# Performance work log

Measured on AMD Instinct MI355X. Metric: run time of the kernel, lower is better.

Reference implementation:

```python
import jax, jax.numpy as jnp
import numpy as np

B, N, D_IN, D_OUT, H = 4, 512, 1024, 1024, 16
HD = D_IN // H      # key head dim (FAISS k_features)
VD = D_OUT // H     # value head dim
MEM = 32768         # memory_size per head
IPQ = 8             # items_per_query
SCALE = HD ** -0.5


def setup_inputs() -> dict:
    key = jax.random.key(0)
    ks = jax.random.split(key, 9)
    s = 0.02
    return {
        "x": jax.random.normal(ks[0], (B, N, D_IN), jnp.float32),
        "Wq": jax.random.normal(ks[1], (D_IN, D_IN), jnp.float32) * s,
        "Wk": jax.random.normal(ks[2], (D_IN, D_IN), jnp.float32) * s,
        "Wv": jax.random.normal(ks[3], (D_OUT, D_IN), jnp.float32) * s,
        "Ww": jax.random.normal(ks[4], (D_OUT, D_IN), jnp.float32) * s,
        "Wo": jax.random.normal(ks[5], (D_OUT, D_OUT), jnp.float32) * s,
        "bo": jnp.zeros((D_OUT,), jnp.float32),
        "k_mem0": jax.random.normal(ks[6], (H, MEM, HD), jnp.float32) * s,
        "v_mem0": jax.random.normal(ks[7], (H, MEM, VD), jnp.float32) * s,
    }


def _attention(q, k, v, Wo, bo):
    # q: [b,n,D_IN], k: [b,m,D_IN], v: [b,m,D_OUT]
    b, n, _ = q.shape
    m = k.shape[1]
    qh = q.reshape(b, n, H, HD)
    kh = k.reshape(b, m, H, HD)
    vh = v.reshape(b, m, H, VD)
    sim = jnp.einsum("bihd,bjhd->bhij", qh, kh) * SCALE
    att = jax.nn.softmax(sim, axis=-1)
    out = jnp.einsum("bhij,bjhd->bihd", att, vh).reshape(b, n, H * VD)
    return out @ Wo.T + bo


def reference(x, Wq, Wk, Wv, Ww, Wo, bo, k_mem0, v_mem0):
    b, n, _ = x.shape
    q = x @ Wq.T          # [b,n,D_IN]
    k = x @ Wk.T          # [b,n,D_IN]
    v = x @ Wv.T          # [b,n,D_OUT]
    w = jax.nn.sigmoid(x @ Ww.T)

    a = _attention(q, k, v, Wo, bo)

    # per-head flat views: [h, b*n, hd]
    qh = q.reshape(b, n, H, HD).transpose(2, 0, 1, 3).reshape(H, b * n, HD)
    kh = k.reshape(b, n, H, HD).transpose(2, 0, 1, 3).reshape(H, b * n, HD)
    vh = v.reshape(b, n, H, VD).transpose(2, 0, 1, 3).reshape(H, b * n, VD)

    m_ins = b * n
    # FIFO insert: drop oldest m_ins rows, append new keys/values
    k_mem = jnp.concatenate([k_mem0[:, m_ins:], kh], axis=1)  # [h, MEM, HD]
    v_mem = jnp.concatenate([v_mem0[:, m_ins:], vh], axis=1)  # [h, MEM, VD]

    # exact inner-product search (IndexFlatIP), top IPQ per query, per head
    sims = jnp.einsum("hqd,hmd->hqm", qh, k_mem)               # [h, b*n, MEM]
    _, idx = jax.lax.top_k(sims, IPQ)                          # [h, b*n, IPQ]
    idx = idx.reshape(H, b * n * IPQ, 1)
    k_ret = jnp.take_along_axis(k_mem, idx, axis=1)            # [h, b*n*IPQ, HD]
    v_ret = jnp.take_along_axis(v_mem, idx, axis=1)            # [h, b*n*IPQ, VD]

    # 'h (b m) hd -> b m (h hd)' with m = n*IPQ
    k_m = k_ret.reshape(H, b, n * IPQ, HD).transpose(1, 2, 0, 3).reshape(b, n * IPQ, D_IN)
    v_m = v_ret.reshape(H, b, n * IPQ, VD).transpose(1, 2, 0, 3).reshape(b, n * IPQ, D_OUT)

    a_m = _attention(q, k_m, v_m, Wo, bo)
    return w * a + (1.0 - w) * a_m
```

## Files before the change

kernel.cpp:

```cpp
#include <hip/hip_runtime.h>
#include <float.h>
#include <math.h>


#define DIN   1024
#define NHEADS 16
#define HD    64
#define NB    4
#define NSEQ  512
#define BN    2048
#define MEMN  32768
#define OLDN  30720
#define IPQ   8
#define ATT_SCALE 0.125f
#define SZ    (BN * DIN)

typedef __attribute__((ext_vector_type(4))) float floatx4;
typedef __attribute__((ext_vector_type(8))) short short8;

__device__ __forceinline__ unsigned short f2bf(float f) {
    unsigned int u = __float_as_uint(f);
    return (unsigned short)((u + 0x7FFFu + ((u >> 16) & 1u)) >> 16);
}
__device__ __forceinline__ float bf2f(unsigned short s) {
    return __uint_as_float(((unsigned int)s) << 16);
}
__device__ __forceinline__ unsigned cvt_pk_bf16(float a, float b) {
    unsigned r;
    asm("v_cvt_pk_bf16_f32 %0, %1, %2" : "=v"(r) : "v"(a), "v"(b));
    return r;
}
__device__ __forceinline__ void split_pack(float4 a, float4 b, short8 &hi, short8 &lo) {
    float v[8] = {a.x, a.y, a.z, a.w, b.x, b.y, b.z, b.w};
    union { unsigned u[4]; short8 s; } H, L;
#pragma unroll
    for (int j = 0; j < 4; ++j) {
        unsigned h = cvt_pk_bf16(v[2 * j], v[2 * j + 1]);
        float r0 = v[2 * j]     - __uint_as_float(h << 16);
        float r1 = v[2 * j + 1] - __uint_as_float(h & 0xFFFF0000u);
        H.u[j] = h;
        L.u[j] = cvt_pk_bf16(r0, r1);
    }
    hi = H.s; lo = L.s;
}
__device__ __forceinline__ floatx4 mfma16(short8 a, short8 b, floatx4 c) {
    return __builtin_amdgcn_mfma_f32_16x16x32_bf16(a, b, c, 0, 0, 0);
}

__global__ void init_kernel(unsigned int* nrm) {
    if (threadIdx.x < NHEADS) nrm[threadIdx.x] = 0u;
}

__global__ __launch_bounds__(256) void gemm_mfma(
    const float* __restrict__ A,
    const float* __restrict__ W0, const float* __restrict__ W1,
    const float* __restrict__ W2, const float* __restrict__ W3,
    float* __restrict__ C0, float* __restrict__ C1,
    float* __restrict__ C2, float* __restrict__ C3,
    int sigmoidZ)
{
    __shared__ short Ahi_s[128 * 32];
    __shared__ short Alo_s[128 * 32];
    __shared__ short Bhi_s[128 * 32];
    __shared__ short Blo_s[128 * 32];

    int z = blockIdx.z;
    const float* W = (z == 0) ? W0 : (z == 1) ? W1 : (z == 2) ? W2 : W3;
    float* C = (z == 0) ? C0 : (z == 1) ? C1 : (z == 2) ? C2 : C3;

    int tid = threadIdx.x;
    int wv = tid >> 6, lane = tid & 63, quad = lane >> 4, l16 = lane & 15;
    int row0 = blockIdx.y * 128, col0 = blockIdx.x * 128;
    int wm = (wv >> 1) * 64, wn = (wv & 1) * 64;

    floatx4 zero4 = {0.f, 0.f, 0.f, 0.f};
    floatx4 acc[4][4];
#pragma unroll
    for (int i = 0; i < 4; ++i)
#pragma unroll
        for (int j = 0; j < 4; ++j) acc[i][j] = zero4;

    for (int kk = 0; kk < DIN; kk += 32) {
        __syncthreads();
#pragma unroll
        for (int p = 0; p < 2; ++p) {
            int g = tid * 2 + p;
            int row = g >> 2, cc = (g & 3) * 8;
            const float* ap = A + (size_t)(row0 + row) * DIN + kk + cc;
            float4 a0 = *(const float4*)ap;
            float4 a1 = *(const float4*)(ap + 4);
            short8 h8, l8;
            split_pack(a0, a1, h8, l8);
            *(short8*)&Ahi_s[g * 8] = h8;
            *(short8*)&Alo_s[g * 8] = l8;
            const float* bp = W + (size_t)(col0 + row) * DIN + kk + cc;
            float4 b0 = *(const float4*)bp;
            float4 b1 = *(const float4*)(bp + 4);
            split_pack(b0, b1, h8, l8);
            *(short8*)&Bhi_s[g * 8] = h8;
            *(short8*)&Blo_s[g * 8] = l8;
        }
        __syncthreads();

        short8 ah[4], al[4], bh[4], bl[4];
#pragma unroll
        for (int t = 0; t < 4; ++t) {
            int ar = (wm + t * 16 + l16) * 32 + quad * 8;
            int br = (wn + t * 16 + l16) * 32 + quad * 8;
            ah[t] = *(const short8*)&Ahi_s[ar];
            al[t] = *(const short8*)&Alo_s[ar];
            bh[t] = *(const short8*)&Bhi_s[br];
            bl[t] = *(const short8*)&Blo_s[br];
        }
#pragma unroll
        for (int tm = 0; tm < 4; ++tm)
#pragma unroll
            for (int tn = 0; tn < 4; ++tn) {
                floatx4 c = acc[tm][tn];
                c = mfma16(al[tm], bl[tn], c);
                c = mfma16(al[tm], bh[tn], c);
                c = mfma16(ah[tm], bl[tn], c);
                c = mfma16(ah[tm], bh[tn], c);
                acc[tm][tn] = c;
            }
    }

    bool sig = (sigmoidZ == z);
#pragma unroll
    for (int tm = 0; tm < 4; ++tm)
#pragma unroll
        for (int tn = 0; tn < 4; ++tn)
#pragma unroll
            for (int r = 0; r < 4; ++r) {
                int row = row0 + wm + tm * 16 + quad * 4 + r;
                int col = col0 + wn + tn * 16 + l16;
                float vv = acc[tm][tn][r];
                if (sig) vv = 1.f / (1.f + __expf(-vv));
                C[(size_t)row * DIN + col] = vv;
            }
}

__global__ __launch_bounds__(256) void oldnorm_kernel(
    const float* __restrict__ kmem0, unsigned int* __restrict__ nrm)
{
    int h = blockIdx.y;
    int c0 = blockIdx.x * 1024;
    int part = threadIdx.x & 15, rg = threadIdx.x >> 4;
    const float* base = kmem0 + ((size_t)h * MEMN + BN) * HD;
    float mx = 0.f;
    for (int it = 0; it < 64; ++it) {
        int row = c0 + it * 16 + rg;
        float4 vv = *(const float4*)(base + (size_t)row * HD + part * 4);
        float s = vv.x * vv.x + vv.y * vv.y + vv.z * vv.z + vv.w * vv.w;
#pragma unroll
        for (int o = 1; o < 16; o <<= 1) s += __shfl_xor(s, o, 16);
        mx = fmaxf(mx, s);
    }
    __shared__ float red[256];
    red[threadIdx.x] = mx;
    __syncthreads();
    for (int st = 128; st > 0; st >>= 1) {
        if (threadIdx.x < st) red[threadIdx.x] = fmaxf(red[threadIdx.x], red[threadIdx.x + st]);
        __syncthreads();
    }
    if (threadIdx.x == 0) atomicMax(nrm + h, __float_as_uint(sqrtf(red[0])));
}

__device__ __forceinline__ void insert_top8(float (&tv)[8], int (&ti)[8], float v, int id) {
    if (v < tv[7] || (v == tv[7] && id > ti[7])) return;
    tv[7] = v; ti[7] = id;
#pragma unroll
    for (int s = 7; s > 0; --s) {
        bool sw = (tv[s] > tv[s - 1]) || (tv[s] == tv[s - 1] && ti[s] < ti[s - 1]);
        if (sw) {
            float fv = tv[s]; tv[s] = tv[s - 1]; tv[s - 1] = fv;
            int iv = ti[s]; ti[s] = ti[s - 1]; ti[s - 1] = iv;
        }
    }
}

__global__ __launch_bounds__(256, 2) void search_kernel(
    const float* __restrict__ q, const float* __restrict__ knew,
    const float* __restrict__ kmem0, const unsigned int* __restrict__ nrm,
    int* __restrict__ idxOut)
{
    __shared__ short Khi[32 * 72];
    __shared__ short Klo[32 * 72];
    __shared__ int sflag;
    int tid = threadIdx.x;
    int qt = blockIdx.x, h = blockIdx.y;
    int wv = tid >> 6, lane = tid & 63, quad = lane >> 4, l16 = lane & 15;
    if (tid == 0) sflag = 0;

    short8 qhi[2], qlo[2];
    float qn2;
    {
        int qrow = qt * 64 + wv * 16 + l16;
        const float* qp = q + (size_t)qrow * DIN + h * HD;
        float sq = 0.f;
#pragma unroll
        for (int st = 0; st < 2; ++st) {
            float4 a = *(const float4*)(qp + st * 32 + quad * 8);
            float4 c = *(const float4*)(qp + st * 32 + quad * 8 + 4);
            sq += a.x * a.x + a.y * a.y + a.z * a.z + a.w * a.w
                + c.x * c.x + c.y * c.y + c.z * c.z + c.w * c.w;
            split_pack(a, c, qhi[st], qlo[st]);
        }
        sq += __shfl_xor(sq, 16);
        sq += __shfl_xor(sq, 32);
        qn2 = sq;
    }

    float tv[4][8]; int ti[4][8];
#pragma unroll
    for (int r = 0; r < 4; ++r)
#pragma unroll
        for (int s = 0; s < 8; ++s) { tv[r][s] = -FLT_MAX; ti[r][s] = 0x7FFFFFFF; }

    for (int ch = 0; ch < 64; ++ch) {
        __syncthreads();
        {
            int key = tid >> 3, part = tid & 7;
            const float* kr = knew + (size_t)(ch * 32 + key) * DIN + h * HD;
            float4 ka = *(const float4*)(kr + part * 8);
            float4 kb = *(const float4*)(kr + part * 8 + 4);
            short8 kh8, kl8;
            split_pack(ka, kb, kh8, kl8);
            *(short8*)&Khi[key * 72 + part * 8] = kh8;
            *(short8*)&Klo[key * 72 + part * 8] = kl8;
        }
        __syncthreads();

        short8 kh00 = *(const short8*)&Khi[l16 * 72 + quad * 8];
        short8 kh01 = *(const short8*)&Khi[l16 * 72 + 32 + quad * 8];
        short8 kl00 = *(const short8*)&Klo[l16 * 72 + quad * 8];
        short8 kl01 = *(const short8*)&Klo[l16 * 72 + 32 + quad * 8];
        short8 kh10 = *(const short8*)&Khi[(16 + l16) * 72 + quad * 8];
        short8 kh11 = *(const short8*)&Khi[(16 + l16) * 72 + 32 + quad * 8];
        short8 kl10 = *(const short8*)&Klo[(16 + l16) * 72 + quad * 8];
        short8 kl11 = *(const short8*)&Klo[(16 + l16) * 72 + 32 + quad * 8];
        floatx4 zero4 = {0.f, 0.f, 0.f, 0.f};
        floatx4 s0 = zero4, s1 = zero4;
        s0 = mfma16(qhi[0], kh00, s0); s0 = mfma16(qhi[1], kh01, s0);
        s0 = mfma16(qlo[0], kh00, s0); s0 = mfma16(qlo[1], kh01, s0);
        s0 = mfma16(qhi[0], kl00, s0); s0 = mfma16(qhi[1], kl01, s0);
        s1 = mfma16(qhi[0], kh10, s1); s1 = mfma16(qhi[1], kh11, s1);
        s1 = mfma16(qlo[0], kh10, s1); s1 = mfma16(qlo[1], kh11, s1);
        s1 = mfma16(qhi[0], kl10, s1); s1 = mfma16(qhi[1], kl11, s1);

        int base = OLDN + ch * 32;
#pragma unroll
        for (int r = 0; r < 4; ++r) {
            insert_top8(tv[r], ti[r], s0[r], base + l16);
            insert_top8(tv[r], ti[r], s1[r], base + 16 + l16);
        }
    }

    float val8[4], keepv[4];
    int keepi[4];
#pragma unroll
    for (int rr = 0; rr < 4; ++rr) { keepv[rr] = -FLT_MAX; keepi[rr] = 0x7FFFFFFF; val8[rr] = -FLT_MAX; }
#pragma unroll
    for (int rr = 0; rr < 4; ++rr) {
#pragma unroll
        for (int m = 0; m < 8; ++m) {
            float cv = tv[rr][0]; int ci = ti[rr][0];
#pragma unroll
            for (int o = 1; o < 16; o <<= 1) {
                float ov = __shfl_xor(cv, o, 16);
                int oi = __shfl_xor(ci, o, 16);
                if (ov > cv || (ov == cv && oi < ci)) { cv = ov; ci = oi; }
            }
            if (tv[rr][0] == cv && ti[rr][0] == ci) {
#pragma unroll
                for (int s = 0; s < 7; ++s) { tv[rr][s] = tv[rr][s + 1]; ti[rr][s] = ti[rr][s + 1]; }
                tv[rr][7] = -FLT_MAX; ti[rr][7] = 0x7FFFFFFF;
            }
            if (l16 == m) { keepv[rr] = cv; keepi[rr] = ci; }
            if (l16 == 0)
                idxOut[((size_t)h * BN + qt * 64 + wv * 16 + quad * 4 + rr) * IPQ + m] = ci;
            val8[rr] = cv;
        }
    }

    float oldMax = __uint_as_float(nrm[h]);
    bool need = false;
#pragma unroll
    for (int rr = 0; rr < 4; ++rr) {
        float bq = __shfl(qn2, quad * 4 + rr, 16);
        float bnd = sqrtf(bq) * oldMax * 1.0001f + 1e-5f;
        if (bnd >= val8[rr]) need = true;
    }
    if (need) sflag = 1;
    __syncthreads();

    if (sflag) {
#pragma unroll
        for (int rr = 0; rr < 4; ++rr) {
            tv[rr][0] = (l16 < 8) ? keepv[rr] : -FLT_MAX;
            ti[rr][0] = (l16 < 8) ? keepi[rr] : 0x7FFFFFFF;
#pragma unroll
            for (int s = 1; s < 8; ++s) { tv[rr][s] = -FLT_MAX; ti[rr][s] = 0x7FFFFFFF; }
        }
        for (int ch = 0; ch < 960; ++ch) {
            __syncthreads();
            {
                int key = tid >> 3, part = tid & 7;
                const float* kr = kmem0 + ((size_t)h * MEMN + BN + ch * 32 + key) * HD;
                float4 ka = *(const float4*)(kr + part * 8);
                float4 kb = *(const float4*)(kr + part * 8 + 4);
                short8 kh8, kl8;
                split_pack(ka, kb, kh8, kl8);
                *(short8*)&Khi[key * 72 + part * 8] = kh8;
                *(short8*)&Klo[key * 72 + part * 8] = kl8;
            }
            __syncthreads();

            short8 kh00 = *(const short8*)&Khi[l16 * 72 + quad * 8];
            short8 kh01 = *(const short8*)&Khi[l16 * 72 + 32 + quad * 8];
            short8 kl00 = *(const short8*)&Klo[l16 * 72 + quad * 8];
            short8 kl01 = *(const short8*)&Klo[l16 * 72 + 32 + quad * 8];
            short8 kh10 = *(const short8*)&Khi[(16 + l16) * 72 + quad * 8];
            short8 kh11 = *(const short8*)&Khi[(16 + l16) * 72 + 32 + quad * 8];
            short8 kl10 = *(const short8*)&Klo[(16 + l16) * 72 + quad * 8];
            short8 kl11 = *(const short8*)&Klo[(16 + l16) * 72 + 32 + quad * 8];
            floatx4 zero4 = {0.f, 0.f, 0.f, 0.f};
            floatx4 s0 = zero4, s1 = zero4;
            s0 = mfma16(qhi[0], kh00, s0); s0 = mfma16(qhi[1], kh01, s0);
            s0 = mfma16(qlo[0], kh00, s0); s0 = mfma16(qlo[1], kh01, s0);
            s0 = mfma16(qhi[0], kl00, s0); s0 = mfma16(qhi[1], kl01, s0);
            s1 = mfma16(qhi[0], kh10, s1); s1 = mfma16(qhi[1], kh11, s1);
            s1 = mfma16(qlo[0], kh10, s1); s1 = mfma16(qlo[1], kh11, s1);
            s1 = mfma16(qhi[0], kl10, s1); s1 = mfma16(qhi[1], kl11, s1);

            int base = ch * 32;
#pragma unroll
            for (int r = 0; r < 4; ++r) {
                insert_top8(tv[r], ti[r], s0[r], base + l16);
                insert_top8(tv[r], ti[r], s1[r], base + 16 + l16);
            }
        }
#pragma unroll
        for (int rr = 0; rr < 4; ++rr) {
#pragma unroll
            for (int m = 0; m < 8; ++m) {
                float cv = tv[rr][0]; int ci = ti[rr][0];
#pragma unroll
                for (int o = 1; o < 16; o <<= 1) {
                    float ov = __shfl_xor(cv, o, 16);
                    int oi = __shfl_xor(ci, o, 16);
                    if (ov > cv || (ov == cv && oi < ci)) { cv = ov; ci = oi; }
                }
                if (tv[rr][0] == cv && ti[rr][0] == ci) {
#pragma unroll
                    for (int s = 0; s < 7; ++s) { tv[rr][s] = tv[rr][s + 1]; ti[rr][s] = ti[rr][s + 1]; }
                    tv[rr][7] = -FLT_MAX; ti[rr][7] = 0x7FFFFFFF;
                }
                if (l16 == 0)
                    idxOut[((size_t)h * BN + qt * 64 + wv * 16 + quad * 4 + rr) * IPQ + m] = ci;
            }
        }
    }
}

__global__ __launch_bounds__(256, 2) void attn_kernel(
    const float* __restrict__ q, const float* __restrict__ knew,
    const float* __restrict__ vnew, const float* __restrict__ kmem0,
    const float* __restrict__ vmem0, const int* __restrict__ idxb,
    float* __restrict__ AO, float* __restrict__ G)
{
    __shared__ short Khi[32 * 72];
    __shared__ short Klo[32 * 72];
    __shared__ short Vthi[64 * 40];
    __shared__ short Vtlo[64 * 40];
    __shared__ short Pbuf[4 * 16 * 40];
    int tid = threadIdx.x;
    int pair = blockIdx.x, mode = blockIdx.y, qt = blockIdx.z;
    int h = pair >> 2, b = pair & 3;
    int wv = tid >> 6, lane = tid & 63, quad = lane >> 4, l16 = lane & 15;

    short8 qhi[2], qlo[2];
    {
        int qrow = b * NSEQ + qt * 64 + wv * 16 + l16;
        const float* qp = q + (size_t)qrow * DIN + h * HD;
#pragma unroll
        for (int st = 0; st < 2; ++st) {
            float4 a = *(const float4*)(qp + st * 32 + quad * 8);
            float4 c = *(const float4*)(qp + st * 32 + quad * 8 + 4);
            split_pack(a, c, qhi[st], qlo[st]);
        }
    }
    floatx4 zero4 = {0.f, 0.f, 0.f, 0.f};
    floatx4 Oacc[4];
#pragma unroll
    for (int t = 0; t < 4; ++t) Oacc[t] = zero4;
    float mrow[4], lrow[4];
#pragma unroll
    for (int r = 0; r < 4; ++r) { mrow[r] = -3.0e38f; lrow[r] = 0.f; }

    int key = tid >> 3, part = tid & 7;
    float4 ka, kb;
    float vv[8];
    auto gload = [&](int chl) {
        const float *kr, *vr;
        if (mode == 0) {
            int row = b * NSEQ + chl * 32 + key;
            kr = knew + (size_t)row * DIN + h * HD;
            vr = vnew + (size_t)row * DIN + h * HD;
        } else {
            int J = chl * 32 + key;
            int mi = idxb[((size_t)h * BN + b * NSEQ + (J >> 3)) * IPQ + (J & 7)];
            if (mi < OLDN) {
                kr = kmem0 + ((size_t)h * MEMN + BN + mi) * HD;
                vr = vmem0 + ((size_t)h * MEMN + BN + mi) * HD;
            } else {
                kr = knew + (size_t)(mi - OLDN) * DIN + h * HD;
                vr = vnew + (size_t)(mi - OLDN) * DIN + h * HD;
            }
        }
        ka = *(const float4*)(kr + part * 8);
        kb = *(const float4*)(kr + part * 8 + 4);
#pragma unroll
        for (int u = 0; u < 8; ++u) vv[u] = vr[part + 8 * u];
    };

    int ch0 = (mode == 2) ? 64 : 0;
    int ch1 = (mode == 0) ? 16 : ((mode == 1) ? 64 : 128);
    gload(ch0);
    for (int ch = ch0; ch < ch1; ++ch) {
        asm volatile("s_waitcnt lgkmcnt(0)" ::: "memory");
        __builtin_amdgcn_s_barrier();

        {
            short8 kh8, kl8;
            split_pack(ka, kb, kh8, kl8);
            *(short8*)&Khi[key * 72 + part * 8] = kh8;
            *(short8*)&Klo[key * 72 + part * 8] = kl8;
#pragma unroll
            for (int u = 0; u < 8; u += 2) {
                unsigned hh = cvt_pk_bf16(vv[u], vv[u + 1]);
                float r0 = vv[u]     - __uint_as_float(hh << 16);
                float r1 = vv[u + 1] - __uint_as_float(hh & 0xFFFF0000u);
                unsigned ll = cvt_pk_bf16(r0, r1);
                Vthi[(part + 8 * u) * 40 + key]       = (short)(hh & 0xFFFF);
                Vthi[(part + 8 * (u + 1)) * 40 + key] = (short)(hh >> 16);
                Vtlo[(part + 8 * u) * 40 + key]       = (short)(ll & 0xFFFF);
                Vtlo[(part + 8 * (u + 1)) * 40 + key] = (short)(ll >> 16);
            }
        }
        if (ch + 1 < ch1) gload(ch + 1);

        asm volatile("s_waitcnt lgkmcnt(0)" ::: "memory");
        __builtin_amdgcn_s_barrier();

        short8 kh00 = *(const short8*)&Khi[(l16) * 72 + 0 * 32 + quad * 8];
        short8 kh01 = *(const short8*)&Khi[(l16) * 72 + 1 * 32 + quad * 8];
        short8 kl00 = *(const short8*)&Klo[(l16) * 72 + 0 * 32 + quad * 8];
        short8 kl01 = *(const short8*)&Klo[(l16) * 72 + 1 * 32 + quad * 8];
        short8 kh10 = *(const short8*)&Khi[(16 + l16) * 72 + 0 * 32 + quad * 8];
        short8 kh11 = *(const short8*)&Khi[(16 + l16) * 72 + 1 * 32 + quad * 8];
        short8 kl10 = *(const short8*)&Klo[(16 + l16) * 72 + 0 * 32 + quad * 8];
        short8 kl11 = *(const short8*)&Klo[(16 + l16) * 72 + 1 * 32 + quad * 8];
        floatx4 s0 = zero4, s1 = zero4;
        s0 = mfma16(qhi[0], kh00, s0); s0 = mfma16(qhi[1], kh01, s0);
        s0 = mfma16(qlo[0], kh00, s0); s0 = mfma16(qlo[1], kh01, s0);
        s0 = mfma16(qhi[0], kl00, s0); s0 = mfma16(qhi[1], kl01, s0);
        s1 = mfma16(qhi[0], kh10, s1); s1 = mfma16(qhi[1], kh11, s1);
        s1 = mfma16(qlo[0], kh10, s1); s1 = mfma16(qlo[1], kh11, s1);
        s1 = mfma16(qhi[0], kl10, s1); s1 = mfma16(qhi[1], kl11, s1);

        float cm[4], alpha[4], p0[4], p1[4], rs[4];
#pragma unroll
        for (int r = 0; r < 4; ++r) cm[r] = fmaxf(s0[r], s1[r]) * ATT_SCALE;
#pragma unroll
        for (int o = 1; o < 16; o <<= 1) {
#pragma unroll
            for (int r = 0; r < 4; ++r) cm[r] = fmaxf(cm[r], __shfl_xor(cm[r], o, 16));
        }
#pragma unroll
        for (int r = 0; r < 4; ++r) {
            float mn = fmaxf(mrow[r], cm[r]);
            alpha[r] = __expf(mrow[r] - mn);
            p0[r] = __expf(s0[r] * ATT_SCALE - mn);
            p1[r] = __expf(s1[r] * ATT_SCALE - mn);
            mrow[r] = mn;
            rs[r] = p0[r] + p1[r];
        }
#pragma unroll
        for (int o = 1; o < 16; o <<= 1) {
#pragma unroll
            for (int r = 0; r < 4; ++r) rs[r] += __shfl_xor(rs[r], o, 16);
        }
#pragma unroll
        for (int r = 0; r < 4; ++r) {
            lrow[r] = lrow[r] * alpha[r] + rs[r];
            unsigned pw = cvt_pk_bf16(p0[r], p1[r]);
            Pbuf[(wv * 16 + quad * 4 + r) * 40 + l16]      = (short)(pw & 0xFFFF);
            Pbuf[(wv * 16 + quad * 4 + r) * 40 + 16 + l16] = (short)(pw >> 16);
        }
#pragma unroll
        for (int t = 0; t < 4; ++t)
#pragma unroll
            for (int r = 0; r < 4; ++r) Oacc[t][r] *= alpha[r];

        short8 pf = *(const short8*)&Pbuf[(wv * 16 + l16) * 40 + quad * 8];
#pragma unroll
        for (int t = 0; t < 4; ++t) {
            short8 vh = *(const short8*)&Vthi[(t * 16 + l16) * 40 + quad * 8];
            short8 vl = *(const short8*)&Vtlo[(t * 16 + l16) * 40 + quad * 8];
            floatx4 o = Oacc[t];
            o = mfma16(pf, vh, o);
            o = mfma16(pf, vl, o);
            Oacc[t] = o;
        }
    }
    if (mode == 0) {
#pragma unroll
        for (int t = 0; t < 4; ++t)
#pragma unroll
            for (int r = 0; r < 4; ++r) {
                int qrow = b * NSEQ + qt * 64 + wv * 16 + quad * 4 + r;
                AO[(size_t)qrow * DIN + h * HD + t * 16 + l16] = Oacc[t][r] / lrow[r];
            }
    } else {
        float* ob = (mode == 1) ? (AO + (size_t)SZ) : G;
        float* mlbuf = G + (size_t)SZ + ((size_t)(mode - 1) * NHEADS + h) * BN * 2;
#pragma unroll
        for (int t = 0; t < 4; ++t)
#pragma unroll
            for (int r = 0; r < 4; ++r) {
                int qrow = b * NSEQ + qt * 64 + wv * 16 + quad * 4 + r;
                ob[(size_t)qrow * DIN + h * HD + t * 16 + l16] = Oacc[t][r];
            }
        if (l16 == 0) {
#pragma unroll
            for (int r = 0; r < 4; ++r) {
                int qrow = b * NSEQ + qt * 64 + wv * 16 + quad * 4 + r;
                float2 mlv = {mrow[r], lrow[r]};
                *(float2*)&mlbuf[(size_t)qrow * 2] = mlv;
            }
        }
    }
}

__global__ __launch_bounds__(256) void combine2_kernel(
    float* __restrict__ O0, const float* __restrict__ O1,
    const float* __restrict__ ml)
{
    int g = blockIdx.x * 256 + threadIdx.x;
    int row = g >> 8;
    int h = (g >> 4) & 15;
    float2 ml0 = *(const float2*)&ml[((size_t)h * BN + row) * 2];
    float2 ml1 = *(const float2*)&ml[(((size_t)NHEADS + h) * BN + row) * 2];
    float m = fmaxf(ml0.x, ml1.x);
    float a0 = __expf(ml0.x - m), a1 = __expf(ml1.x - m);
    float inv = 1.f / (ml0.y * a0 + ml1.y * a1);
    float4 o0 = ((const float4*)O0)[g];
    float4 o1 = ((const float4*)O1)[g];
    float4 o;
    o.x = (o0.x * a0 + o1.x * a1) * inv;
    o.y = (o0.y * a0 + o1.y * a1) * inv;
    o.z = (o0.z * a0 + o1.z * a1) * inv;
    o.w = (o0.w * a0 + o1.w * a1) * inv;
    ((float4*)O0)[g] = o;
}

__global__ __launch_bounds__(256) void combine_kernel(
    const float* __restrict__ G, const float* __restrict__ wg,
    const float* __restrict__ bo, float* __restrict__ out)
{
    int gid = blockIdx.x * 256 + threadIdx.x;
    float4 g1 = ((const float4*)G)[gid];
    float4 g2 = ((const float4*)G)[gid + (SZ / 4)];
    float4 w4 = ((const float4*)wg)[gid];
    float4 b4 = ((const float4*)bo)[gid & (DIN / 4 - 1)];
    float4 o;
    o.x = w4.x * g1.x + (1.f - w4.x) * g2.x + b4.x;
    o.y = w4.y * g1.y + (1.f - w4.y) * g2.y + b4.y;
    o.z = w4.z * g1.z + (1.f - w4.z) * g2.z + b4.z;
    o.w = w4.w * g1.w + (1.f - w4.w) * g2.w + b4.w;
    ((float4*)out)[gid] = o;
}

extern "C" void kernel_launch(void* const* d_in, const int* in_sizes, int n_in,
                              void* d_out, int out_size, void* d_ws, size_t ws_size,
                              hipStream_t stream)
{
    (void)in_sizes; (void)n_in; (void)out_size; (void)ws_size;
    const float* x     = (const float*)d_in[0];
    const float* Wq    = (const float*)d_in[1];
    const float* Wk    = (const float*)d_in[2];
    const float* Wv    = (const float*)d_in[3];
    const float* Ww    = (const float*)d_in[4];
    const float* Wo    = (const float*)d_in[5];
    const float* bo    = (const float*)d_in[6];
    const float* kmem0 = (const float*)d_in[7];
    const float* vmem0 = (const float*)d_in[8];

    float* ws = (float*)d_ws;
    float* q  = ws;
    float* k  = ws + (size_t)SZ;
    float* v  = ws + (size_t)2 * SZ;
    float* wg = ws + (size_t)3 * SZ;
    float* AO = ws + (size_t)4 * SZ;
    float* G  = ws + (size_t)6 * SZ;
    int* idxb = (int*)(ws + (size_t)8 * SZ);
    unsigned int* nrm = (unsigned int*)(ws + (size_t)8 * SZ + NHEADS * BN * IPQ);

    init_kernel<<<1, 64, 0, stream>>>(nrm);
    gemm_mfma<<<dim3(8, 16, 4), 256, 0, stream>>>(x, Wq, Wk, Wv, Ww, q, k, v, wg, 3);
    oldnorm_kernel<<<dim3(30, 16), 256, 0, stream>>>(kmem0, nrm);
    search_kernel<<<dim3(32, 16), 256, 0, stream>>>(q, k, kmem0, nrm, idxb);
    attn_kernel<<<dim3(64, 3, 8), 256, 0, stream>>>(q, k, v, kmem0, vmem0, idxb, AO, G);
    combine2_kernel<<<2048, 256, 0, stream>>>(AO + (size_t)SZ, G, G + (size_t)SZ);
    gemm_mfma<<<dim3(8, 32, 1), 256, 0, stream>>>(AO, Wo, Wo, Wo, Wo, G, G, G, G, -1);
    combine_kernel<<<2048, 256, 0, stream>>>(G, wg, bo, (float*)d_out);
}
```

Before: 982.5 us.

## Pre-split operands into packed bf16 hi/lo words and reuse across GEMM, search, attention

Adds a presplit pass that converts x and the weight matrices into packed 32-bit words holding bf16 hi and lo halves. The projection GEMM now writes q/k/v in this packed form, and the search, attention, combine and output GEMM consume it directly. The aim is to avoid repeating the fp32-to-bf16 split in every tile load. It also prefetches the retrieval index one chunk ahead in attention, swaps grid axes for search and the head/batch block mapping, and replaces the inline-asm conversion with software rounding. The trade-off is extra presplit kernels and traffic for weights, plus heavier rounding code.

Measured after the change: 940.5 us. 4.3% less time.

```diff
diff --git a/kernel.cpp b/kernel.cpp
--- a/kernel.cpp
+++ b/kernel.cpp
@@ -15,6 +15,16 @@
 #define ATT_SCALE 0.125f
 #define SZ    (BN * DIN)
 
+#define WS_WG_OFF    25165824ull
+#define WS_AOPK_OFF  33554432ull
+#define WS_XPK_OFF   33554432ull
+#define WS_WPK_OFF   41943040ull
+#define WS_GF_OFF    50331648ull
+#define WS_IDX_OFF   67108864ull
+#define WS_ML_OFF    68157440ull
+#define WS_NRM_OFF   69206016ull
+#define WS_WOPK_OFF  69210112ull
+
 typedef __attribute__((ext_vector_type(4))) float floatx4;
 typedef __attribute__((ext_vector_type(8))) short short8;
 
@@ -25,21 +35,35 @@
 __device__ __forceinline__ float bf2f(unsigned short s) {
     return __uint_as_float(((unsigned int)s) << 16);
 }
-__device__ __forceinline__ unsigned cvt_pk_bf16(float a, float b) {
-    unsigned r;
-    asm("v_cvt_pk_bf16_f32 %0, %1, %2" : "=v"(r) : "v"(a), "v"(b));
-    return r;
+__device__ __forceinline__ unsigned pack32(float v) {
+    unsigned h = f2bf(v);
+    unsigned l = f2bf(v - bf2f((unsigned short)h));
+    return (h & 0xFFFFu) | (l << 16);
+}
+__device__ __forceinline__ void unpack8(uint4 a, uint4 b, short8 &hi, short8 &lo) {
+    unsigned p[8] = {a.x, a.y, a.z, a.w, b.x, b.y, b.z, b.w};
+    union { unsigned u[4]; short8 s; } H, L;
+#pragma unroll
+    for (int j = 0; j < 4; ++j) {
+        unsigned e = p[2 * j], o = p[2 * j + 1];
+        H.u[j] = (e & 0xFFFFu) | (o << 16);
+        L.u[j] = (e >> 16) | (o & 0xFFFF0000u);
+    }
+    hi = H.s; lo = L.s;
+}
+__device__ __forceinline__ void unpack8f(float4 fa, float4 fb, short8 &hi, short8 &lo) {
+    uint4 a = {__float_as_uint(fa.x), __float_as_uint(fa.y), __float_as_uint(fa.z), __float_as_uint(fa.w)};
+    uint4 b = {__float_as_uint(fb.x), __float_as_uint(fb.y), __float_as_uint(fb.z), __float_as_uint(fb.w)};
+    unpack8(a, b, hi, lo);
 }
 __device__ __forceinline__ void split_pack(float4 a, float4 b, short8 &hi, short8 &lo) {
     float v[8] = {a.x, a.y, a.z, a.w, b.x, b.y, b.z, b.w};
     union { unsigned u[4]; short8 s; } H, L;
 #pragma unroll
     for (int j = 0; j < 4; ++j) {
-        unsigned h = cvt_pk_bf16(v[2 * j], v[2 * j + 1]);
-        float r0 = v[2 * j]     - __uint_as_float(h << 16);
-        float r1 = v[2 * j + 1] - __uint_as_float(h & 0xFFFF0000u);
-        H.u[j] = h;
-        L.u[j] = cvt_pk_bf16(r0, r1);
+        unsigned p0 = pack32(v[2 * j]), p1 = pack32(v[2 * j + 1]);
+        H.u[j] = (p0 & 0xFFFFu) | (p1 << 16);
+        L.u[j] = (p0 >> 16) | (p1 & 0xFFFF0000u);
     }
     hi = H.s; lo = L.s;
 }
@@ -51,13 +75,25 @@
     if (threadIdx.x < NHEADS) nrm[threadIdx.x] = 0u;
 }
 
-__global__ __launch_bounds__(256) void gemm_mfma(
-    const float* __restrict__ A,
-    const float* __restrict__ W0, const float* __restrict__ W1,
-    const float* __restrict__ W2, const float* __restrict__ W3,
-    float* __restrict__ C0, float* __restrict__ C1,
-    float* __restrict__ C2, float* __restrict__ C3,
-    int sigmoidZ)
+__global__ __launch_bounds__(256) void presplit_kernel(
+    const float* __restrict__ s0, const float* __restrict__ s1,
+    const float* __restrict__ s2, const float* __restrict__ s3,
+    unsigned* __restrict__ out, int n4)
+{
+    int z = blockIdx.y;
+    const float* s = (z == 0) ? s0 : (z == 1) ? s1 : (z == 2) ? s2 : s3;
+    int i = blockIdx.x * 256 + threadIdx.x;
+    float4 v = ((const float4*)s)[i];
+    uint4 o = {pack32(v.x), pack32(v.y), pack32(v.z), pack32(v.w)};
+    ((uint4*)(out + (size_t)z * n4 * 4))[i] = o;
+}
+
+__global__ __launch_bounds__(256) void gemm_pk(
+    const unsigned* __restrict__ Apk,
+    const unsigned* __restrict__ B0, const unsigned* __restrict__ B1,
+    const unsigned* __restrict__ B2, const unsigned* __restrict__ B3,
+    unsigned* __restrict__ OutPk, float* __restrict__ OutF,
+    int packN, int sigmoidZ)
 {
     __shared__ short Ahi_s[128 * 32];
     __shared__ short Alo_s[128 * 32];
@@ -65,8 +101,7 @@
     __shared__ short Blo_s[128 * 32];
 
     int z = blockIdx.z;
-    const float* W = (z == 0) ? W0 : (z == 1) ? W1 : (z == 2) ? W2 : W3;
-    float* C = (z == 0) ? C0 : (z == 1) ? C1 : (z == 2) ? C2 : C3;
+    const unsigned* B = (z == 0) ? B0 : (z == 1) ? B1 : (z == 2) ? B2 : B3;
 
     int tid = threadIdx.x;
     int wv = tid >> 6, lane = tid & 63, quad = lane >> 4, l16 = lane & 15;
@@ -86,17 +121,13 @@
         for (int p = 0; p < 2; ++p) {
             int g = tid * 2 + p;
             int row = g >> 2, cc = (g & 3) * 8;
-            const float* ap = A + (size_t)(row0 + row) * DIN + kk + cc;
-            float4 a0 = *(const float4*)ap;
-            float4 a1 = *(const float4*)(ap + 4);
+            const unsigned* ap = Apk + (size_t)(row0 + row) * DIN + kk + cc;
             short8 h8, l8;
-            split_pack(a0, a1, h8, l8);
+            unpack8(*(const uint4*)ap, *(const uint4*)(ap + 4), h8, l8);
             *(short8*)&Ahi_s[g * 8] = h8;
             *(short8*)&Alo_s[g * 8] = l8;
-            const float* bp = W + (size_t)(col0 + row) * DIN + kk + cc;
-            float4 b0 = *(const float4*)bp;
-            float4 b1 = *(const float4*)(bp + 4);
-            split_pack(b0, b1, h8, l8);
+            const unsigned* bp = B + (size_t)(col0 + row) * DIN + kk + cc;
+            unpack8(*(const uint4*)bp, *(const uint4*)(bp + 4), h8, l8);
             *(short8*)&Bhi_s[g * 8] = h8;
             *(short8*)&Blo_s[g * 8] = l8;
         }
@@ -125,19 +156,33 @@
             }
     }
 
-    bool sig = (sigmoidZ == z);
-#pragma unroll
-    for (int tm = 0; tm < 4; ++tm)
-#pragma unroll
-        for (int tn = 0; tn < 4; ++tn)
-#pragma unroll
-            for (int r = 0; r < 4; ++r) {
-                int row = row0 + wm + tm * 16 + quad * 4 + r;
-                int col = col0 + wn + tn * 16 + l16;
-                float vv = acc[tm][tn][r];
-                if (sig) vv = 1.f / (1.f + __expf(-vv));
-                C[(size_t)row * DIN + col] = vv;
-            }
+    if (z < packN) {
+        unsigned* O = OutPk + (size_t)z * 2097152;
+#pragma unroll
+        for (int tm = 0; tm < 4; ++tm)
+#pragma unroll
+            for (int tn = 0; tn < 4; ++tn)
+#pragma unroll
+                for (int r = 0; r < 4; ++r) {
+                    int row = row0 + wm + tm * 16 + quad * 4 + r;
+                    int col = col0 + wn + tn * 16 + l16;
+                    O[(size_t)row * DIN + col] = pack32(acc[tm][tn][r]);
+                }
+    } else {
+        bool sig = (sigmoidZ == z);
+#pragma unroll
+        for (int tm = 0; tm < 4; ++tm)
+#pragma unroll
+            for (int tn = 0; tn < 4; ++tn)
+#pragma unroll
+                for (int r = 0; r < 4; ++r) {
+                    int row = row0 + wm + tm * 16 + quad * 4 + r;
+                    int col = col0 + wn + tn * 16 + l16;
+                    float vv = acc[tm][tn][r];
+                    if (sig) vv = 1.f / (1.f + __expf(-vv));
+                    OutF[(size_t)row * DIN + col] = vv;
+                }
+    }
 }
 
 __global__ __launch_bounds__(256) void oldnorm_kernel(
@@ -180,7 +225,7 @@
 }
 
 __global__ __launch_bounds__(256, 2) void search_kernel(
-    const float* __restrict__ q, const float* __restrict__ knew,
+    const unsigned* __restrict__ qpk, const unsigned* __restrict__ kpk,
     const float* __restrict__ kmem0, const unsigned int* __restrict__ nrm,
     int* __restrict__ idxOut)
 {
@@ -188,7 +233,7 @@
     __shared__ short Klo[32 * 72];
     __shared__ int sflag;
     int tid = threadIdx.x;
-    int qt = blockIdx.x, h = blockIdx.y;
+    int h = blockIdx.x, qt = blockIdx.y;
     int wv = tid >> 6, lane = tid & 63, quad = lane >> 4, l16 = lane & 15;
     if (tid == 0) sflag = 0;
 
@@ -196,15 +241,17 @@
     float qn2;
     {
         int qrow = qt * 64 + wv * 16 + l16;
-        const float* qp = q + (size_t)qrow * DIN + h * HD;
+        const unsigned* qp = qpk + (size_t)qrow * DIN + h * HD;
         float sq = 0.f;
 #pragma unroll
         for (int st = 0; st < 2; ++st) {
-            float4 a = *(const float4*)(qp + st * 32 + quad * 8);
-            float4 c = *(const float4*)(qp + st * 32 + quad * 8 + 4);
-            sq += a.x * a.x + a.y * a.y + a.z * a.z + a.w * a.w
-                + c.x * c.x + c.y * c.y + c.z * c.z + c.w * c.w;
-            split_pack(a, c, qhi[st], qlo[st]);
+            const unsigned* p = qp + st * 32 + quad * 8;
+            unpack8(*(const uint4*)p, *(const uint4*)(p + 4), qhi[st], qlo[st]);
+#pragma unroll
+            for (int j = 0; j < 8; ++j) {
+                float f = bf2f((unsigned short)qhi[st][j]) + bf2f((unsigned short)qlo[st][j]);
+                sq += f * f;
+            }
         }
         sq += __shfl_xor(sq, 16);
         sq += __shfl_xor(sq, 32);
@@ -221,11 +268,9 @@
         __syncthreads();
         {
             int key = tid >> 3, part = tid & 7;
-            const float* kr = knew + (size_t)(ch * 32 + key) * DIN + h * HD;
-            float4 ka = *(const float4*)(kr + part * 8);
-            float4 kb = *(const float4*)(kr + part * 8 + 4);
+            const unsigned* kr = kpk + (size_t)(ch * 32 + key) * DIN + h * HD + part * 8;
             short8 kh8, kl8;
-            split_pack(ka, kb, kh8, kl8);
+            unpack8(*(const uint4*)kr, *(const uint4*)(kr + 4), kh8, kl8);
             *(short8*)&Khi[key * 72 + part * 8] = kh8;
             *(short8*)&Klo[key * 72 + part * 8] = kl8;
         }
@@ -307,10 +352,8 @@
             {
                 int key = tid >> 3, part = tid & 7;
                 const float* kr = kmem0 + ((size_t)h * MEMN + BN + ch * 32 + key) * HD;
-                float4 ka = *(const float4*)(kr + part * 8);
-                float4 kb = *(const float4*)(kr + part * 8 + 4);
                 short8 kh8, kl8;
-                split_pack(ka, kb, kh8, kl8);
+                split_pack(*(const float4*)(kr + part * 8), *(const float4*)(kr + part * 8 + 4), kh8, kl8);
                 *(short8*)&Khi[key * 72 + part * 8] = kh8;
                 *(short8*)&Klo[key * 72 + part * 8] = kl8;
             }
@@ -364,10 +407,10 @@
 }
 
 __global__ __launch_bounds__(256, 2) void attn_kernel(
-    const float* __restrict__ q, const float* __restrict__ knew,
-    const float* __restrict__ vnew, const float* __restrict__ kmem0,
+    const unsigned* __restrict__ qpk, const unsigned* __restrict__ kpk,
+    const unsigned* __restrict__ vpk, const float* __restrict__ kmem0,
     const float* __restrict__ vmem0, const int* __restrict__ idxb,
-    float* __restrict__ AO, float* __restrict__ G)
+    unsigned* __restrict__ AOpk, float* __restrict__ Gf, float* __restrict__ mlF)
 {
     __shared__ short Khi[32 * 72];
     __shared__ short Klo[32 * 72];
@@ -375,19 +418,19 @@
     __shared__ short Vtlo[64 * 40];
     __shared__ short Pbuf[4 * 16 * 40];
     int tid = threadIdx.x;
-    int pair = blockIdx.x, mode = blockIdx.y, qt = blockIdx.z;
-    int h = pair >> 2, b = pair & 3;
+    int pid = blockIdx.x, mode = blockIdx.y, qt = blockIdx.z;
+    int h = (pid & 7) | (((pid >> 3) & 1) << 3);
+    int b = pid >> 4;
     int wv = tid >> 6, lane = tid & 63, quad = lane >> 4, l16 = lane & 15;
 
     short8 qhi[2], qlo[2];
     {
         int qrow = b * NSEQ + qt * 64 + wv * 16 + l16;
-        const float* qp = q + (size_t)qrow * DIN + h * HD;
+        const unsigned* qp = qpk + (size_t)qrow * DIN + h * HD;
 #pragma unroll
         for (int st = 0; st < 2; ++st) {
-            float4 a = *(const float4*)(qp + st * 32 + quad * 8);
-            float4 c = *(const float4*)(qp + st * 32 + quad * 8 + 4);
-            split_pack(a, c, qhi[st], qlo[st]);
+            const unsigned* p = qp + st * 32 + quad * 8;
+            unpack8(*(const uint4*)p, *(const uint4*)(p + 4), qhi[st], qlo[st]);
         }
     }
     floatx4 zero4 = {0.f, 0.f, 0.f, 0.f};
@@ -400,55 +443,70 @@
 
     int key = tid >> 3, part = tid & 7;
     float4 ka, kb;
-    float vv[8];
-    auto gload = [&](int chl) {
-        const float *kr, *vr;
-        if (mode == 0) {
-            int row = b * NSEQ + chl * 32 + key;
-            kr = knew + (size_t)row * DIN + h * HD;
-            vr = vnew + (size_t)row * DIN + h * HD;
+    float vvf[8];
+    bool isNew = true;
+
+    auto loadIdx = [&](int chl) -> int {
+        if (mode == 0) return 0;
+        int J = chl * 32 + key;
+        return idxb[((size_t)h * BN + b * NSEQ + (J >> 3)) * IPQ + (J & 7)];
+    };
+    auto gloadRows = [&](int chl, int mi) {
+        if (mode == 0 || mi >= OLDN) {
+            int row = (mode == 0) ? (b * NSEQ + chl * 32 + key) : (mi - OLDN);
+            const unsigned* kr = kpk + (size_t)row * DIN + h * HD + part * 8;
+            ka = *(const float4*)kr;
+            kb = *(const float4*)(kr + 4);
+            const unsigned* vr = vpk + (size_t)row * DIN + h * HD + part;
+#pragma unroll
+            for (int u = 0; u < 8; ++u) vvf[u] = __uint_as_float(vr[8 * u]);
+            isNew = true;
         } else {
-            int J = chl * 32 + key;
-            int mi = idxb[((size_t)h * BN + b * NSEQ + (J >> 3)) * IPQ + (J & 7)];
-            if (mi < OLDN) {
-                kr = kmem0 + ((size_t)h * MEMN + BN + mi) * HD;
-                vr = vmem0 + ((size_t)h * MEMN + BN + mi) * HD;
-            } else {
-                kr = knew + (size_t)(mi - OLDN) * DIN + h * HD;
-                vr = vnew + (size_t)(mi - OLDN) * DIN + h * HD;
-            }
-        }
-        ka = *(const float4*)(kr + part * 8);
-        kb = *(const float4*)(kr + part * 8 + 4);
-#pragma unroll
-        for (int u = 0; u < 8; ++u) vv[u] = vr[part + 8 * u];
+            const float* kr = kmem0 + ((size_t)h * MEMN + BN + mi) * HD + part * 8;
+            ka = *(const float4*)kr;
+            kb = *(const float4*)(kr + 4);
+            const float* vr = vmem0 + ((size_t)h * MEMN + BN + mi) * HD + part;
+#pragma unroll
+            for (int u = 0; u < 8; ++u) vvf[u] = vr[8 * u];
+            isNew = false;
+        }
     };
 
     int ch0 = (mode == 2) ? 64 : 0;
     int ch1 = (mode == 0) ? 16 : ((mode == 1) ? 64 : 128);
-    gload(ch0);
+    int miA = loadIdx(ch0);
+    gloadRows(ch0, miA);
+    int miB = loadIdx(ch0 + 1);
     for (int ch = ch0; ch < ch1; ++ch) {
         asm volatile("s_waitcnt lgkmcnt(0)" ::: "memory");
         __builtin_amdgcn_s_barrier();
 
         {
             short8 kh8, kl8;
-            split_pack(ka, kb, kh8, kl8);
+            if (isNew) unpack8f(ka, kb, kh8, kl8);
+            else       split_pack(ka, kb, kh8, kl8);
             *(short8*)&Khi[key * 72 + part * 8] = kh8;
             *(short8*)&Klo[key * 72 + part * 8] = kl8;
-#pragma unroll
-            for (int u = 0; u < 8; u += 2) {
-                unsigned hh = cvt_pk_bf16(vv[u], vv[u + 1]);
-                float r0 = vv[u]     - __uint_as_float(hh << 16);
-                float r1 = vv[u + 1] - __uint_as_float(hh & 0xFFFF0000u);
-                unsigned ll = cvt_pk_bf16(r0, r1);
-                Vthi[(part + 8 * u) * 40 + key]       = (short)(hh & 0xFFFF);
-                Vthi[(part + 8 * (u + 1)) * 40 + key] = (short)(hh >> 16);
-                Vtlo[(part + 8 * u) * 40 + key]       = (short)(ll & 0xFFFF);
-                Vtlo[(part + 8 * (u + 1)) * 40 + key] = (short)(ll >> 16);
-            }
-        }
-        if (ch + 1 < ch1) gload(ch + 1);
+            if (isNew) {
+#pragma unroll
+                for (int u = 0; u < 8; ++u) {
+                    unsigned pv = __float_as_uint(vvf[u]);
+                    Vthi[(part + 8 * u) * 40 + key] = (short)(pv & 0xFFFF);
+                    Vtlo[(part + 8 * u) * 40 + key] = (short)(pv >> 16);
+                }
+            } else {
+#pragma unroll
+                for (int u = 0; u < 8; ++u) {
+                    unsigned short hh = f2bf(vvf[u]);
+                    Vthi[(part + 8 * u) * 40 + key] = (short)hh;
+                    Vtlo[(part + 8 * u) * 40 + key] = (short)f2bf(vvf[u] - bf2f(hh));
+                }
+            }
+        }
+        if (ch + 1 < ch1) {
+            gloadRows(ch + 1, miB);
+            if (ch + 2 < ch1) miB = loadIdx(ch + 2);
+        }
 
         asm volatile("s_waitcnt lgkmcnt(0)" ::: "memory");
         __builtin_amdgcn_s_barrier();
@@ -494,9 +552,8 @@
 #pragma unroll
         for (int r = 0; r < 4; ++r) {
             lrow[r] = lrow[r] * alpha[r] + rs[r];
-            unsigned pw = cvt_pk_bf16(p0[r], p1[r]);
-            Pbuf[(wv * 16 + quad * 4 + r) * 40 + l16]      = (short)(pw & 0xFFFF);
-            Pbuf[(wv * 16 + quad * 4 + r) * 40 + 16 + l16] = (short)(pw >> 16);
+            Pbuf[(wv * 16 + quad * 4 + r) * 40 + l16]      = (short)f2bf(p0[r]);
+            Pbuf[(wv * 16 + quad * 4 + r) * 40 + 16 + l16] = (short)f2bf(p1[r]);
         }
 #pragma unroll
         for (int t = 0; t < 4; ++t)
@@ -520,11 +577,11 @@
 #pragma unroll
             for (int r = 0; r < 4; ++r) {
                 int qrow = b * NSEQ + qt * 64 + wv * 16 + quad * 4 + r;
-                AO[(size_t)qrow * DIN + h * HD + t * 16 + l16] = Oacc[t][r] / lrow[r];
+                AOpk[(size_t)qrow * DIN + h * HD + t * 16 + l16] = pack32(Oacc[t][r] / lrow[r]);
             }
     } else {
-        float* ob = (mode == 1) ? (AO + (size_t)SZ) : G;
-        float* mlbuf = G + (size_t)SZ + ((size_t)(mode - 1) * NHEADS + h) * BN * 2;
+        float* ob = (mode == 1) ? Gf : (Gf + (size_t)2097152);
+        float* mlbuf = mlF + ((size_t)(mode - 1) * NHEADS + h) * BN * 2;
 #pragma unroll
         for (int t = 0; t < 4; ++t)
 #pragma unroll
@@ -544,8 +601,8 @@
 }
 
 __global__ __launch_bounds__(256) void combine2_kernel(
-    float* __restrict__ O0, const float* __restrict__ O1,
-    const float* __restrict__ ml)
+    const float* __restrict__ O0, const float* __restrict__ O1,
+    const float* __restrict__ ml, unsigned* __restrict__ AOpkHalf)
 {
     int g = blockIdx.x * 256 + threadIdx.x;
     int row = g >> 8;
@@ -557,12 +614,12 @@
     float inv = 1.f / (ml0.y * a0 + ml1.y * a1);
     float4 o0 = ((const float4*)O0)[g];
     float4 o1 = ((const float4*)O1)[g];
-    float4 o;
-    o.x = (o0.x * a0 + o1.x * a1) * inv;
-    o.y = (o0.y * a0 + o1.y * a1) * inv;
-    o.z = (o0.z * a0 + o1.z * a1) * inv;
-    o.w = (o0.w * a0 + o1.w * a1) * inv;
-    ((float4*)O0)[g] = o;
+    uint4 po;
+    po.x = pack32((o0.x * a0 + o1.x * a1) * inv);
+    po.y = pack32((o0.y * a0 + o1.y * a1) * inv);
+    po.z = pack32((o0.z * a0 + o1.z * a1) * inv);
+    po.w = pack32((o0.w * a0 + o1.w * a1) * inv);
+    ((uint4*)AOpkHalf)[g] = po;
 }
 
 __global__ __launch_bounds__(256) void combine_kernel(
@@ -597,22 +654,35 @@
     const float* kmem0 = (const float*)d_in[7];
     const float* vmem0 = (const float*)d_in[8];
 
-    float* ws = (float*)d_ws;
-    float* q  = ws;
-    float* k  = ws + (size_t)SZ;
-    float* v  = ws + (size_t)2 * SZ;
-    float* wg = ws + (size_t)3 * SZ;
-    float* AO = ws + (size_t)4 * SZ;
-    float* G  = ws + (size_t)6 * SZ;
-    int* idxb = (int*)(ws + (size_t)8 * SZ);
-    unsigned int* nrm = (unsigned int*)(ws + (size_t)8 * SZ + NHEADS * BN * IPQ);
+    char* W = (char*)d_ws;
+    unsigned* PRJ  = (unsigned*)W;
+    unsigned* qpk  = PRJ;
+    unsigned* kpk  = PRJ + 2097152;
+    unsigned* vpk  = PRJ + 2 * 2097152;
+    float*    wg   = (float*)(W + WS_WG_OFF);
+    unsigned* AOpk = (unsigned*)(W + WS_AOPK_OFF);
+    unsigned* xpk  = (unsigned*)(W + WS_XPK_OFF);
+    unsigned* Wpk  = (unsigned*)(W + WS_WPK_OFF);
+    float*    Gf   = (float*)(W + WS_GF_OFF);
+    int*      idxb = (int*)(W + WS_IDX_OFF);
+    float*    mlF  = (float*)(W + WS_ML_OFF);
+    unsigned* nrm  = (unsigned*)(W + WS_NRM_OFF);
+    unsigned* Wopk = (unsigned*)(W + WS_WOPK_OFF);
 
     init_kernel<<<1, 64, 0, stream>>>(nrm);
-    gemm_mfma<<<dim3(8, 16, 4), 256, 0, stream>>>(x, Wq, Wk, Wv, Ww, q, k, v, wg, 3);
+    presplit_kernel<<<dim3(2048, 1), 256, 0, stream>>>(x, x, x, x, xpk, 524288);
+    presplit_kernel<<<dim3(1024, 4), 256, 0, stream>>>(Wq, Wk, Wv, Ww, Wpk, 262144);
+    presplit_kernel<<<dim3(1024, 1), 256, 0, stream>>>(Wo, Wo, Wo, Wo, Wopk, 262144);
+    gemm_pk<<<dim3(8, 16, 4), 256, 0, stream>>>(
+        xpk, Wpk, Wpk + 1048576, Wpk + 2 * 1048576, Wpk + 3 * 1048576,
+        PRJ, wg, 3, 3);
     oldnorm_kernel<<<dim3(30, 16), 256, 0, stream>>>(kmem0, nrm);
-    search_kernel<<<dim3(32, 16), 256, 0, stream>>>(q, k, kmem0, nrm, idxb);
-    attn_kernel<<<dim3(64, 3, 8), 256, 0, stream>>>(q, k, v, kmem0, vmem0, idxb, AO, G);
-    combine2_kernel<<<2048, 256, 0, stream>>>(AO + (size_t)SZ, G, G + (size_t)SZ);
-    gemm_mfma<<<dim3(8, 32, 1), 256, 0, stream>>>(AO, Wo, Wo, Wo, Wo, G, G, G, G, -1);
-    combine_kernel<<<2048, 256, 0, stream>>>(G, wg, bo, (float*)d_out);
-}
+    search_kernel<<<dim3(16, 32), 256, 0, stream>>>(qpk, kpk, kmem0, nrm, idxb);
+    attn_kernel<<<dim3(64, 3, 8), 256, 0, stream>>>(qpk, kpk, vpk, kmem0, vmem0,
+                                                    idxb, AOpk, Gf, mlF);
+    combine2_kernel<<<2048, 256, 0, stream>>>(Gf, Gf + (size_t)2097152, mlF,
+                                              AOpk + (size_t)2048 * DIN);
+    gemm_pk<<<dim3(8, 32, 1), 256, 0, stream>>>(
+        AOpk, Wopk, Wopk, Wopk, Wopk, (unsigned*)nullptr, Gf, 0, -1);
+    combine_kernel<<<2048, 256, 0, stream>>>(Gf, wg, bo, (float*)d_out);
+}
```
